# Kernel tuning notes

Measured on AMD Instinct MI355X. Metric: run time of the kernel, lower is better.

The kernel has to match this reference:

```python
import jax, jax.numpy as jnp
import numpy as np

N_NODES = 100000


def gcn_conv(x, row, col, W, b, n_nodes):
    # PyG GCNConv: add self-loops, symmetric normalization, linear, scatter-add, bias
    deg = jnp.zeros((n_nodes,), x.dtype).at[col].add(1.0)
    dinv = jnp.where(deg > 0, jax.lax.rsqrt(deg), 0.0)
    norm = dinv[row] * dinv[col]                      # [E+N]
    h = x @ W                                         # [N, out]
    msg = h[row] * norm[:, None]                      # [E+N, out]
    out = jax.ops.segment_sum(msg, col, num_segments=n_nodes)
    return out + b


def setup_inputs() -> dict:
    key = jax.random.key(0)
    ks = jax.random.split(key, 8)
    E = 1600000
    edge_index = jax.random.randint(ks[0], (2, E), 0, N_NODES, dtype=jnp.int64)
    node_features = jax.random.normal(ks[1], (N_NODES, 16), dtype=jnp.float32)
    W1 = jax.random.normal(ks[2], (16, 32), dtype=jnp.float32) * 0.25
    b1 = jnp.zeros((32,), jnp.float32)
    W2 = jax.random.normal(ks[3], (32, 16), dtype=jnp.float32) * 0.18
    b2 = jnp.zeros((16,), jnp.float32)
    fc_W = jax.random.normal(ks[4], (16, 1), dtype=jnp.float32) * 0.25
    fc_b = jnp.zeros((1,), jnp.float32)
    return {"edge_index": edge_index, "node_features": node_features,
            "W1": W1, "b1": b1, "W2": W2, "b2": b2, "fc_W": fc_W, "fc_b": fc_b}


def reference(edge_index, node_features, W1, b1, W2, b2, fc_W, fc_b):
    n = node_features.shape[0]
    loops = jnp.arange(n, dtype=edge_index.dtype)
    row = jnp.concatenate([edge_index[0], loops])     # sources (with self-loops)
    col = jnp.concatenate([edge_index[1], loops])     # targets (with self-loops)
    x = jax.nn.relu(gcn_conv(node_features, row, col, W1, b1, n))
    # F.dropout with training=False is identity (inference)
    x = jax.nn.relu(gcn_conv(x, row, col, W2, b2, n))
    return x @ fc_W + fc_b
```

## Files before the change

kernel.cpp:

```cpp
#include <hip/hip_runtime.h>
#include <hip/hip_fp16.h>


constexpr int NN  = 100000;
constexpr int FIN = 16;
constexpr int FH  = 32;
constexpr int FO  = 16;

constexpr int BK      = 256;
constexpr int NBUCKET = (NN + BK - 1) / BK;
constexpr int CHUNK   = 4096;
constexpr int CAP     = 5376;

static __device__ __forceinline__ int pack2(float a, float b) {
    __half2 t = __float22half2_rn(make_float2(a, b));
    return *reinterpret_cast<int*>(&t);
}
static __device__ __forceinline__ float2 unpack2(int v) {
    __half2 t = *reinterpret_cast<__half2*>(&v);
    return __half22float2(t);
}

__global__ void init_kernel(int* __restrict__ bcursor) {
    int b = blockIdx.x * blockDim.x + threadIdx.x;
    if (b < NBUCKET) bcursor[b] = b * CAP;
}

__global__ __launch_bounds__(256) void bucket_fill_kernel(
        const int* __restrict__ row, const int* __restrict__ col,
        int* __restrict__ bcursor, int* __restrict__ srow, int E) {
    __shared__ int bcnt[NBUCKET];
    __shared__ int bcur[NBUCKET];
    int t = threadIdx.x;
    int e0 = blockIdx.x * CHUNK;
    int m = E - e0; if (m > CHUNK) m = CHUNK;
    for (int b = t; b < NBUCKET; b += 256) bcnt[b] = 0;
    __syncthreads();
    for (int i = t; i < m; i += 256)
        atomicAdd(&bcnt[col[e0 + i] >> 8], 1);
    __syncthreads();
    for (int b = t; b < NBUCKET; b += 256) {
        int v = bcnt[b];
        bcur[b] = v ? atomicAdd(&bcursor[b], v) : 0;
    }
    __syncthreads();
    for (int i = t; i < m; i += 256) {
        int c = col[e0 + i];
        int r = row[e0 + i];
        int p = atomicAdd(&bcur[c >> 8], 1);
        srow[p] = ((c & (BK - 1)) << 17) | r;
    }
}

__global__ __launch_bounds__(256) void bucket_sort_mm1_kernel(
        const int* __restrict__ bcursor, int* __restrict__ srow,
        int2* __restrict__ offcnt, float* __restrict__ dinv,
        const float* __restrict__ x, const float* __restrict__ W1,
        __half* __restrict__ g1, int n) {
    __shared__ int sorted[CAP];
    __shared__ int cnt2[BK];
    __shared__ int aux[BK];
    __shared__ float w1[FIN * FH];
    int t = threadIdx.x;
    for (int i = t; i < FIN * FH; i += 256) w1[i] = W1[i];
    int lo = blockIdx.x << 8;
    int nodes = n - lo; if (nodes > BK) nodes = BK;
    int s0 = blockIdx.x * CAP;
    int m = bcursor[blockIdx.x] - s0;
    if (m > CAP) m = CAP;
    cnt2[t] = 0;
    __syncthreads();
    for (int i = t; i < m; i += 256) atomicAdd(&cnt2[srow[s0 + i] >> 17], 1);
    __syncthreads();
    int v = cnt2[t];
    aux[t] = v;
    __syncthreads();
    for (int d = 1; d < BK; d <<= 1) {
        int a = (t >= d) ? aux[t - d] : 0;
        __syncthreads();
        aux[t] += a;
        __syncthreads();
    }
    int excl = aux[t] - v;
    cnt2[t] = excl;
    float di = rsqrtf((float)v + 1.0f);
    if (t < nodes) {
        offcnt[lo + t] = make_int2(s0 + excl, v);
        dinv[lo + t]   = di;
    }
    __syncthreads();
    for (int i = t; i < m; i += 256) {
        int pv = srow[s0 + i];
        int p = atomicAdd(&cnt2[pv >> 17], 1);
        sorted[p] = pv & 0x1FFFF;
    }
    __syncthreads();
    for (int i = t; i < m; i += 256) srow[s0 + i] = sorted[i];
    if (t < nodes) {
        int nd = lo + t;
        float xi[FIN];
        const float4* xv = (const float4*)(x + (long long)nd * FIN);
        #pragma unroll
        for (int i = 0; i < FIN / 4; i++) {
            float4 vv = xv[i];
            xi[4*i] = vv.x; xi[4*i+1] = vv.y; xi[4*i+2] = vv.z; xi[4*i+3] = vv.w;
        }
        float h[FH];
        #pragma unroll
        for (int j = 0; j < FH; j++) h[j] = 0.f;
        #pragma unroll
        for (int i = 0; i < FIN; i++) {
            float xs = xi[i];
            #pragma unroll
            for (int j = 0; j < FH; j++) h[j] += xs * w1[i * FH + j];
        }
        int4* gv = (int4*)(g1 + (long long)nd * FH);
        #pragma unroll
        for (int k = 0; k < 4; k++) {
            gv[k] = make_int4(pack2(h[8*k]*di,   h[8*k+1]*di),
                              pack2(h[8*k+2]*di, h[8*k+3]*di),
                              pack2(h[8*k+4]*di, h[8*k+5]*di),
                              pack2(h[8*k+6]*di, h[8*k+7]*di));
        }
    }
}

constexpr int XS = 36;
__global__ __launch_bounds__(256) void gather_mm2_kernel(
        const int2* __restrict__ offcnt,
        const int* __restrict__ srow, const __half* __restrict__ g1,
        const float* __restrict__ dinv, const float* __restrict__ b1,
        const float* __restrict__ W2, __half* __restrict__ g2, int n) {
    __shared__ float xs[64 * XS];
    __shared__ float w[FH * FO];
    __shared__ float bb[FH];
    int t = threadIdx.x;
    for (int i = t; i < FH * FO; i += 256) w[i] = W2[i];
    if (t < FH) bb[t] = b1[t];
    int nl = t >> 2;
    int q = t & 3;
    int node = blockIdx.x * 64 + nl;
    bool live = node < n;
    float acc[8] = {0.f,0.f,0.f,0.f,0.f,0.f,0.f,0.f};
    float di = 0.f;
    if (live) {
        di = dinv[node];
        {
            int4 raw = ((const int4*)(g1 + (long long)node * FH))[q];
            float2 f0 = unpack2(raw.x), f1 = unpack2(raw.y);
            float2 f2 = unpack2(raw.z), f3 = unpack2(raw.w);
            acc[0] = f0.x; acc[1] = f0.y; acc[2] = f1.x; acc[3] = f1.y;
            acc[4] = f2.x; acc[5] = f2.y; acc[6] = f3.x; acc[7] = f3.y;
        }
        int2 oc = offcnt[node];
        int s = oc.x, m = oc.y;
        int i = 0;
        for (; i + 3 < m; i += 4) {
            int r0 = srow[s + i];
            int r1 = srow[s + i + 1];
            int r2 = srow[s + i + 2];
            int r3 = srow[s + i + 3];
            int4 ra = ((const int4*)(g1 + (long long)r0 * FH))[q];
            int4 rb = ((const int4*)(g1 + (long long)r1 * FH))[q];
            int4 rc = ((const int4*)(g1 + (long long)r2 * FH))[q];
            int4 rd = ((const int4*)(g1 + (long long)r3 * FH))[q];
            float2 u;
            u = unpack2(ra.x); acc[0] += u.x; acc[1] += u.y;
            u = unpack2(ra.y); acc[2] += u.x; acc[3] += u.y;
            u = unpack2(ra.z); acc[4] += u.x; acc[5] += u.y;
            u = unpack2(ra.w); acc[6] += u.x; acc[7] += u.y;
            u = unpack2(rb.x); acc[0] += u.x; acc[1] += u.y;
            u = unpack2(rb.y); acc[2] += u.x; acc[3] += u.y;
            u = unpack2(rb.z); acc[4] += u.x; acc[5] += u.y;
            u = unpack2(rb.w); acc[6] += u.x; acc[7] += u.y;
            u = unpack2(rc.x); acc[0] += u.x; acc[1] += u.y;
            u = unpack2(rc.y); acc[2] += u.x; acc[3] += u.y;
            u = unpack2(rc.z); acc[4] += u.x; acc[5] += u.y;
            u = unpack2(rc.w); acc[6] += u.x; acc[7] += u.y;
            u = unpack2(rd.x); acc[0] += u.x; acc[1] += u.y;
            u = unpack2(rd.y); acc[2] += u.x; acc[3] += u.y;
            u = unpack2(rd.z); acc[4] += u.x; acc[5] += u.y;
            u = unpack2(rd.w); acc[6] += u.x; acc[7] += u.y;
        }
        for (; i < m; i++) {
            int r0 = srow[s + i];
            int4 ra = ((const int4*)(g1 + (long long)r0 * FH))[q];
            float2 u;
            u = unpack2(ra.x); acc[0] += u.x; acc[1] += u.y;
            u = unpack2(ra.y); acc[2] += u.x; acc[3] += u.y;
            u = unpack2(ra.z); acc[4] += u.x; acc[5] += u.y;
            u = unpack2(ra.w); acc[6] += u.x; acc[7] += u.y;
        }
    }
    __syncthreads();
    if (live) {
        float* xr = xs + nl * XS + 8 * q;
        #pragma unroll
        for (int j = 0; j < 8; j++) {
            float a = acc[j] * di + bb[8*q + j];
            xr[j] = a > 0.f ? a : 0.f;
        }
    }
    __syncthreads();
    if (live) {
        const float* xr = xs + nl * XS;
        int k0 = 4 * q;
        float o0 = 0.f, o1 = 0.f, o2 = 0.f, o3 = 0.f;
        #pragma unroll
        for (int j = 0; j < FH; j++) {
            float xj = xr[j];
            const float* wr = w + j * FO + k0;
            o0 += xj * wr[0];
            o1 += xj * wr[1];
            o2 += xj * wr[2];
            o3 += xj * wr[3];
        }
        ((int2*)(g2 + (long long)node * FO))[q] =
            make_int2(pack2(o0 * di, o1 * di), pack2(o2 * di, o3 * di));
    }
}

__global__ __launch_bounds__(256) void gather_fc_kernel(
        const int2* __restrict__ offcnt,
        const int* __restrict__ srow, const __half* __restrict__ g2,
        const float* __restrict__ dinv, const float* __restrict__ b2,
        const float* __restrict__ fcW, const float* __restrict__ fcb,
        float* __restrict__ out, int n) {
    __shared__ float w[FO];
    __shared__ float bb[FO];
    __shared__ float fb;
    int t = threadIdx.x;
    if (t < FO) { w[t] = fcW[t]; bb[t] = b2[t]; }
    if (t == 0) fb = fcb[0];
    __syncthreads();
    int node = blockIdx.x * 128 + (t >> 1);
    int q = t & 1;
    if (node >= n) return;
    float di = dinv[node];
    float acc[8];
    {
        int4 raw = ((const int4*)(g2 + (long long)node * FO))[q];
        float2 f0 = unpack2(raw.x), f1 = unpack2(raw.y);
        float2 f2 = unpack2(raw.z), f3 = unpack2(raw.w);
        acc[0] = f0.x; acc[1] = f0.y; acc[2] = f1.x; acc[3] = f1.y;
        acc[4] = f2.x; acc[5] = f2.y; acc[6] = f3.x; acc[7] = f3.y;
    }
    int2 oc = offcnt[node];
    int s = oc.x, m = oc.y;
    int i = 0;
    for (; i + 3 < m; i += 4) {
        int r0 = srow[s + i];
        int r1 = srow[s + i + 1];
        int r2 = srow[s + i + 2];
        int r3 = srow[s + i + 3];
        int4 ra = ((const int4*)(g2 + (long long)r0 * FO))[q];
        int4 rb = ((const int4*)(g2 + (long long)r1 * FO))[q];
        int4 rc = ((const int4*)(g2 + (long long)r2 * FO))[q];
        int4 rd = ((const int4*)(g2 + (long long)r3 * FO))[q];
        float2 u;
        u = unpack2(ra.x); acc[0] += u.x; acc[1] += u.y;
        u = unpack2(ra.y); acc[2] += u.x; acc[3] += u.y;
        u = unpack2(ra.z); acc[4] += u.x; acc[5] += u.y;
        u = unpack2(ra.w); acc[6] += u.x; acc[7] += u.y;
        u = unpack2(rb.x); acc[0] += u.x; acc[1] += u.y;
        u = unpack2(rb.y); acc[2] += u.x; acc[3] += u.y;
        u = unpack2(rb.z); acc[4] += u.x; acc[5] += u.y;
        u = unpack2(rb.w); acc[6] += u.x; acc[7] += u.y;
        u = unpack2(rc.x); acc[0] += u.x; acc[1] += u.y;
        u = unpack2(rc.y); acc[2] += u.x; acc[3] += u.y;
        u = unpack2(rc.z); acc[4] += u.x; acc[5] += u.y;
        u = unpack2(rc.w); acc[6] += u.x; acc[7] += u.y;
        u = unpack2(rd.x); acc[0] += u.x; acc[1] += u.y;
        u = unpack2(rd.y); acc[2] += u.x; acc[3] += u.y;
        u = unpack2(rd.z); acc[4] += u.x; acc[5] += u.y;
        u = unpack2(rd.w); acc[6] += u.x; acc[7] += u.y;
    }
    for (; i < m; i++) {
        int r0 = srow[s + i];
        int4 ra = ((const int4*)(g2 + (long long)r0 * FO))[q];
        float2 u;
        u = unpack2(ra.x); acc[0] += u.x; acc[1] += u.y;
        u = unpack2(ra.y); acc[2] += u.x; acc[3] += u.y;
        u = unpack2(ra.z); acc[4] += u.x; acc[5] += u.y;
        u = unpack2(ra.w); acc[6] += u.x; acc[7] += u.y;
    }
    float p = 0.f;
    #pragma unroll
    for (int j = 0; j < 8; j++) {
        float a = acc[j] * di + bb[8*q + j];
        p += (a > 0.f ? a : 0.f) * w[8*q + j];
    }
    p += __shfl_down(p, 1, 2);
    if (q == 0) out[node] = p + fb;
}

extern "C" void kernel_launch(void* const* d_in, const int* in_sizes, int n_in,
                              void* d_out, int out_size, void* d_ws, size_t ws_size,
                              hipStream_t stream) {
    const int*   edge = (const int*)d_in[0];
    const float* x    = (const float*)d_in[1];
    const float* W1   = (const float*)d_in[2];
    const float* b1   = (const float*)d_in[3];
    const float* W2   = (const float*)d_in[4];
    const float* b2   = (const float*)d_in[5];
    const float* fcW  = (const float*)d_in[6];
    const float* fcb  = (const float*)d_in[7];
    float* out = (float*)d_out;

    const int E = in_sizes[0] / 2;
    const int n = NN;
    const int* row = edge;
    const int* col = edge + E;

    const size_t nA = (size_t)((n + 127) & ~127);
    char* wsb = (char*)d_ws;
    int2*  offcnt  = (int2*)wsb;
    float* dinv    = (float*)(offcnt + nA);
    int*   bcursor = (int*)(dinv + nA);
    int*   srow    = bcursor + 512;
    int*   srowEnd = srow + (size_t)(NBUCKET + 1) * CAP;
    __half* g1     = (__half*)srowEnd;
    __half* g2     = g1 + (size_t)n * FH;

    const int B = 256;
    const int nChunkBlocks = (E + CHUNK - 1) / CHUNK;

    init_kernel<<<2, B, 0, stream>>>(bcursor);
    bucket_fill_kernel<<<nChunkBlocks, B, 0, stream>>>(row, col, bcursor, srow, E);
    bucket_sort_mm1_kernel<<<NBUCKET, B, 0, stream>>>(bcursor, srow, offcnt, dinv, x, W1, g1, n);
    gather_mm2_kernel<<<(n + 63) / 64, B, 0, stream>>>(offcnt, srow, g1, dinv, b1, W2, g2, n);
    gather_fc_kernel<<<(n + 127) / 128, B, 0, stream>>>(offcnt, srow, g2, dinv, b2, fcW, fcb, out, n);
}
```

Baseline: 156.1 us.

## Degree-sort nodes within buckets for balanced gather, stage edges in LDS

Inside each 256-node bucket the sort kernel builds a per-bucket permutation that groups nodes by in-degree (capped at 63) with a small histogram and scan. The two gather kernels then walk nodes through this permutation, so neighbouring lanes in a wavefront have similar edge counts and less divergence. The bucket's edges are also copied once into shared memory instead of being read from global memory twice, and the fill chunk size is doubled. The cost is an extra permutation array, one more indirection per node, more shared memory per block, and scattered per-node output writes.

```diff
diff --git a/kernel.cpp b/kernel.cpp
--- a/kernel.cpp
+++ b/kernel.cpp
@@ -9,7 +9,8 @@
 
 constexpr int BK      = 256;
 constexpr int NBUCKET = (NN + BK - 1) / BK;
-constexpr int CHUNK   = 4096;
+constexpr int NSLOT   = NBUCKET * BK;
+constexpr int CHUNK   = 8192;
 constexpr int CAP     = 5376;
 
 static __device__ __forceinline__ int pack2(float a, float b) {
@@ -55,22 +56,28 @@
 __global__ __launch_bounds__(256) void bucket_sort_mm1_kernel(
         const int* __restrict__ bcursor, int* __restrict__ srow,
         int2* __restrict__ offcnt, float* __restrict__ dinv,
+        int* __restrict__ perm,
         const float* __restrict__ x, const float* __restrict__ W1,
         __half* __restrict__ g1, int n) {
+    __shared__ int ebuf[CAP];
     __shared__ int sorted[CAP];
     __shared__ int cnt2[BK];
     __shared__ int aux[BK];
+    __shared__ int dh[64];
+    __shared__ int dbase[64];
     __shared__ float w1[FIN * FH];
     int t = threadIdx.x;
     for (int i = t; i < FIN * FH; i += 256) w1[i] = W1[i];
+    if (t < 64) dh[t] = 0;
     int lo = blockIdx.x << 8;
     int nodes = n - lo; if (nodes > BK) nodes = BK;
     int s0 = blockIdx.x * CAP;
     int m = bcursor[blockIdx.x] - s0;
     if (m > CAP) m = CAP;
+    for (int i = t; i < m; i += 256) ebuf[i] = srow[s0 + i];
     cnt2[t] = 0;
     __syncthreads();
-    for (int i = t; i < m; i += 256) atomicAdd(&cnt2[srow[s0 + i] >> 17], 1);
+    for (int i = t; i < m; i += 256) atomicAdd(&cnt2[ebuf[i] >> 17], 1);
     __syncthreads();
     int v = cnt2[t];
     aux[t] = v;
@@ -88,9 +95,24 @@
         offcnt[lo + t] = make_int2(s0 + excl, v);
         dinv[lo + t]   = di;
     }
+    int dv = (t < nodes) ? (v > 63 ? 63 : v) : 0;
+    atomicAdd(&dh[dv], 1);
+    __syncthreads();
+    if (t < 64) aux[t] = dh[t];
+    __syncthreads();
+    for (int d = 1; d < 64; d <<= 1) {
+        int a = (t >= d && t < 64) ? aux[t - d] : 0;
+        __syncthreads();
+        if (t < 64) aux[t] += a;
+        __syncthreads();
+    }
+    if (t < 64) { dbase[t] = aux[t] - dh[t]; dh[t] = 0; }
+    __syncthreads();
+    int rank = dbase[dv] + atomicAdd(&dh[dv], 1);
+    perm[lo + rank] = (t < nodes) ? (lo + t) : -1;
     __syncthreads();
     for (int i = t; i < m; i += 256) {
-        int pv = srow[s0 + i];
+        int pv = ebuf[i];
         int p = atomicAdd(&cnt2[pv >> 17], 1);
         sorted[p] = pv & 0x1FFFF;
     }
@@ -127,10 +149,10 @@
 
 constexpr int XS = 36;
 __global__ __launch_bounds__(256) void gather_mm2_kernel(
-        const int2* __restrict__ offcnt,
+        const int2* __restrict__ offcnt, const int* __restrict__ perm,
         const int* __restrict__ srow, const __half* __restrict__ g1,
         const float* __restrict__ dinv, const float* __restrict__ b1,
-        const float* __restrict__ W2, __half* __restrict__ g2, int n) {
+        const float* __restrict__ W2, __half* __restrict__ g2) {
     __shared__ float xs[64 * XS];
     __shared__ float w[FH * FO];
     __shared__ float bb[FH];
@@ -139,8 +161,8 @@
     if (t < FH) bb[t] = b1[t];
     int nl = t >> 2;
     int q = t & 3;
-    int node = blockIdx.x * 64 + nl;
-    bool live = node < n;
+    int node = perm[blockIdx.x * 64 + nl];
+    bool live = node >= 0;
     float acc[8] = {0.f,0.f,0.f,0.f,0.f,0.f,0.f,0.f};
     float di = 0.f;
     if (live) {
@@ -221,11 +243,11 @@
 }
 
 __global__ __launch_bounds__(256) void gather_fc_kernel(
-        const int2* __restrict__ offcnt,
+        const int2* __restrict__ offcnt, const int* __restrict__ perm,
         const int* __restrict__ srow, const __half* __restrict__ g2,
         const float* __restrict__ dinv, const float* __restrict__ b2,
         const float* __restrict__ fcW, const float* __restrict__ fcb,
-        float* __restrict__ out, int n) {
+        float* __restrict__ out) {
     __shared__ float w[FO];
     __shared__ float bb[FO];
     __shared__ float fb;
@@ -233,9 +255,9 @@
     if (t < FO) { w[t] = fcW[t]; bb[t] = b2[t]; }
     if (t == 0) fb = fcb[0];
     __syncthreads();
-    int node = blockIdx.x * 128 + (t >> 1);
+    int node = perm[blockIdx.x * 128 + (t >> 1)];
     int q = t & 1;
-    if (node >= n) return;
+    if (node < 0) return;
     float di = dinv[node];
     float acc[8];
     {
@@ -316,7 +338,8 @@
     char* wsb = (char*)d_ws;
     int2*  offcnt  = (int2*)wsb;
     float* dinv    = (float*)(offcnt + nA);
-    int*   bcursor = (int*)(dinv + nA);
+    int*   perm    = (int*)(dinv + nA);
+    int*   bcursor = perm + ((NSLOT + 127) & ~127);
     int*   srow    = bcursor + 512;
     int*   srowEnd = srow + (size_t)(NBUCKET + 1) * CAP;
     __half* g1     = (__half*)srowEnd;
@@ -327,7 +350,7 @@
 
     init_kernel<<<2, B, 0, stream>>>(bcursor);
     bucket_fill_kernel<<<nChunkBlocks, B, 0, stream>>>(row, col, bcursor, srow, E);
-    bucket_sort_mm1_kernel<<<NBUCKET, B, 0, stream>>>(bcursor, srow, offcnt, dinv, x, W1, g1, n);
-    gather_mm2_kernel<<<(n + 63) / 64, B, 0, stream>>>(offcnt, srow, g1, dinv, b1, W2, g2, n);
-    gather_fc_kernel<<<(n + 127) / 128, B, 0, stream>>>(offcnt, srow, g2, dinv, b2, fcW, fcb, out, n);
-}
+    bucket_sort_mm1_kernel<<<NBUCKET, B, 0, stream>>>(bcursor, srow, offcnt, dinv, perm, x, W1, g1, n);
+    gather_mm2_kernel<<<NSLOT / 64, B, 0, stream>>>(offcnt, perm, srow, g1, dinv, b1, W2, g2);
+    gather_fc_kernel<<<NSLOT / 128, B, 0, stream>>>(offcnt, perm, srow, g2, dinv, b2, fcW, fcb, out);
+}
```

Result: slower. 164.6 us (+5.4%).
